# Optimization experiments

Measured on AMD Instinct MI355X. Metric: run time of the kernel, lower is better.

Reference implementation:

```python
import jax, jax.numpy as jnp
import numpy as np

EPS = 1e-4  # epsilon init kwarg


def setup_inputs() -> dict:
    key = jax.random.key(0)
    a = jax.random.normal(key, (8192, 64, 64), dtype=jnp.float32)
    # module assumes symmetric input (tf.self_adjoint_eig)
    x = 0.5 * (a + a.transpose(0, 2, 1))
    return {"x": x}


def reference(x):
    # batched symmetric eigendecomposition
    s, u = jnp.linalg.eigh(x)            # s: [b, d], u: [b, d, d]
    s = jnp.maximum(s, EPS)              # eigenvalue ReLU with shift epsilon
    # reconstruct: u @ diag(s) @ u^T
    return jnp.einsum('bik,bk,bjk->bij', u, s, u)
```

## Files before the change

### kernel.cpp

```cpp
#include <hip/hip_runtime.h>
#include <cstdint>


#define EPSV 1e-4f

typedef short bf16x8  __attribute__((ext_vector_type(8)));
typedef short short4v __attribute__((ext_vector_type(4)));
typedef float f32x4   __attribute__((ext_vector_type(4)));

__device__ __forceinline__ short f2bf(float f) {
  unsigned u = __float_as_uint(f);
  return (short)((u + 0x7FFFu + ((u >> 16) & 1u)) >> 16);
}
__device__ __forceinline__ float bf2f(short s) {
  return __uint_as_float(((unsigned)(unsigned short)s) << 16);
}
__device__ __forceinline__ int swz(int row, int byte) { return byte ^ ((row & 7) << 4); }

__device__ __forceinline__ bf16x8 ldfrag(const short* S, int row, int kb) {
  return *(const bf16x8*)((const char*)S + swz(row, row * 128 + kb));
}

__device__ __forceinline__ float blockReduceSum(float v, float* red) {
  #pragma unroll
  for (int o = 32; o >= 1; o >>= 1) v += __shfl_xor(v, o, 64);
  const int t = threadIdx.x;
  __syncthreads();
  if ((t & 63) == 0) red[t >> 6] = v;
  __syncthreads();
  return red[0] + red[1] + red[2] + red[3];
}

__device__ __forceinline__ void mm_split(const short* Ph, const short* Pl,
                                         const short* Qh, const short* Ql,
                                         int Rb, int Cb, int l15, int kg,
                                         f32x4 acc[2][2]) {
  #pragma unroll
  for (int mi = 0; mi < 2; mi++)
    #pragma unroll
    for (int ni = 0; ni < 2; ni++) acc[mi][ni] = (f32x4){0.f, 0.f, 0.f, 0.f};
  #pragma unroll
  for (int ks = 0; ks < 2; ks++) {
    const int kb = 64 * ks + 16 * kg;
    bf16x8 ah0 = ldfrag(Ph, Rb + l15,      kb);
    bf16x8 ah1 = ldfrag(Ph, Rb + 16 + l15, kb);
    bf16x8 al0 = ldfrag(Pl, Rb + l15,      kb);
    bf16x8 al1 = ldfrag(Pl, Rb + 16 + l15, kb);
    bf16x8 bh0 = ldfrag(Qh, Cb + l15,      kb);
    bf16x8 bh1 = ldfrag(Qh, Cb + 16 + l15, kb);
    bf16x8 bl0 = ldfrag(Ql, Cb + l15,      kb);
    bf16x8 bl1 = ldfrag(Ql, Cb + 16 + l15, kb);
#define MM(mi, ni, A, B) acc[mi][ni] = __builtin_amdgcn_mfma_f32_16x16x32_bf16(A, B, acc[mi][ni], 0, 0, 0)
    MM(0,0,ah0,bh0); MM(0,0,ah0,bl0); MM(0,0,al0,bh0);
    MM(0,1,ah0,bh1); MM(0,1,ah0,bl1); MM(0,1,al0,bh1);
    MM(1,0,ah1,bh0); MM(1,0,ah1,bl0); MM(1,0,al1,bh0);
    MM(1,1,ah1,bh1); MM(1,1,ah1,bl1); MM(1,1,al1,bh1);
#undef MM
  }
}

__device__ __forceinline__ void writeSym(short* Dh, short* Dl, const f32x4 vals[2][2],
                                         int Rb, int Cb, int l15, int kg, float scale) {
  #pragma unroll
  for (int mi = 0; mi < 2; mi++)
    #pragma unroll
    for (int ni = 0; ni < 2; ni++) {
      const int rp = Cb + 16 * ni + l15;
      const int cb2 = (Rb + 16 * mi + 4 * kg) * 2;
      short4v h, l;
      #pragma unroll
      for (int r = 0; r < 4; r++) {
        float v = vals[mi][ni][r] * scale;
        short hh = f2bf(v);
        h[r] = hh;
        l[r] = f2bf(v - bf2f(hh));
      }
      const int off = swz(rp, rp * 128 + cb2);
      *(short4v*)((char*)Dh + off) = h;
      *(short4v*)((char*)Dl + off) = l;
    }
}

__device__ __forceinline__ void readSym(const short* Sh, const short* Sl,
                                        int Rb, int Cb, int l15, int kg,
                                        f32x4 out[2][2]) {
  #pragma unroll
  for (int mi = 0; mi < 2; mi++)
    #pragma unroll
    for (int ni = 0; ni < 2; ni++) {
      const int rp = Cb + 16 * ni + l15;
      const int off = swz(rp, rp * 128 + (Rb + 16 * mi + 4 * kg) * 2);
      short4v h = *(const short4v*)((const char*)Sh + off);
      short4v l = *(const short4v*)((const char*)Sl + off);
      #pragma unroll
      for (int r = 0; r < 4; r++) out[mi][ni][r] = bf2f(h[r]) + bf2f(l[r]);
    }
}

__global__ __launch_bounds__(256, 2) void mrelu_mfma(const float* __restrict__ X,
                                                     float* __restrict__ O) {
  __shared__ short Yh[4096], Yl[4096], Zh[4096], Zl[4096],
                   Uh[4096], Ul[4096], Wh[4096], Wl[4096];
  __shared__ float red[4];

  const int t = threadIdx.x;
  const int lane = t & 63, wid = t >> 6;
  const int l15 = lane & 15, kg = lane >> 4;
  const int Rb = (wid >> 1) * 32, Cb = (wid & 1) * 32;
  const size_t base = (size_t)blockIdx.x * 4096;
  const float* Xb = X + base;

  float4 ld[4];
  float ssq = 0.f;
  #pragma unroll
  for (int q = 0; q < 4; q++) {
    float4 v = reinterpret_cast<const float4*>(Xb)[t + 256 * q];
    const int e = 4 * t + 1024 * q;
    const int row = e >> 6, col = e & 63;
    const int d = row - col;
    if (d >= 0 && d < 4) (&v.x)[d] -= EPSV;
    ssq += v.x * v.x + v.y * v.y + v.z * v.z + v.w * v.w;
    ld[q] = v;
  }
  const float s0sq = blockReduceSum(ssq, red);
  const float S0 = sqrtf(s0sq) + 1e-30f;
  const float invS0 = 1.0f / S0;

  #pragma unroll
  for (int q = 0; q < 4; q++) {
    const int e = 4 * t + 1024 * q;
    const int row = e >> 6, col = e & 63;
    short4v h, l;
    #pragma unroll
    for (int i = 0; i < 4; i++) {
      float v = (&ld[q].x)[i] * invS0;
      short hh = f2bf(v);
      h[i] = hh;
      l[i] = f2bf(v - bf2f(hh));
    }
    const int off = swz(row, row * 128 + col * 2);
    *(short4v*)((char*)Yh + off) = h;
    *(short4v*)((char*)Yl + off) = l;
  }
  __syncthreads();

  f32x4 acc[2][2];
  mm_split(Yh, Yl, Yh, Yl, Rb, Cb, l15, kg, acc);
  float zss = 0.f;
  #pragma unroll
  for (int mi = 0; mi < 2; mi++)
    #pragma unroll
    for (int ni = 0; ni < 2; ni++)
      #pragma unroll
      for (int r = 0; r < 4; r++) zss += acc[mi][ni][r] * acc[mi][ni][r];
  const float znSq = blockReduceSum(zss, red);
  const float rr = sqrtf(sqrtf(znSq + 1e-30f));
  const float invr = 1.0f / rr;
  const float S = S0 * rr;
  writeSym(Zh, Zl, acc, Rb, Cb, l15, kg, invr * invr);

  {
    f32x4 yv[2][2];
    readSym(Yh, Yl, Rb, Cb, l15, kg, yv);
    #pragma unroll
    for (int mi = 0; mi < 2; mi++)
      #pragma unroll
      for (int ni = 0; ni < 2; ni++)
        #pragma unroll
        for (int r = 0; r < 4; r++) yv[mi][ni][r] *= invr;
    writeSym(Yh, Yl, yv, Rb, Cb, l15, kg, 1.0f);
    writeSym(Wh, Wl, yv, Rb, Cb, l15, kg, 1.0f);
  }
  __syncthreads();

  const float qa = 3.4445f, qb = -4.7750f, qc = 2.0315f;
  #pragma unroll 1
  for (int it = 0; it < 4; it++) {
    mm_split(Zh, Zl, Yh, Yl, Rb, Cb, l15, kg, acc);
    writeSym(Uh, Ul, acc, Rb, Cb, l15, kg, 1.0f);
    __syncthreads();
    mm_split(Zh, Zl, Uh, Ul, Rb, Cb, l15, kg, acc);
    f32x4 yv[2][2], uv[2][2];
    readSym(Yh, Yl, Rb, Cb, l15, kg, yv);
    readSym(Uh, Ul, Rb, Cb, l15, kg, uv);
    f32x4 res[2][2];
    #pragma unroll
    for (int mi = 0; mi < 2; mi++)
      #pragma unroll
      for (int ni = 0; ni < 2; ni++)
        #pragma unroll
        for (int r = 0; r < 4; r++)
          res[mi][ni][r] = qa * yv[mi][ni][r] + qb * uv[mi][ni][r] + qc * acc[mi][ni][r];
    writeSym(Yh, Yl, res, Rb, Cb, l15, kg, 1.0f);
    __syncthreads();
    mm_split(Yh, Yl, Yh, Yl, Rb, Cb, l15, kg, acc);
    writeSym(Zh, Zl, acc, Rb, Cb, l15, kg, 1.0f);
    __syncthreads();
  }

  #pragma unroll 1
  for (int it = 0; it < 3; it++) {
    mm_split(Zh, Zl, Yh, Yl, Rb, Cb, l15, kg, acc);
    f32x4 yv[2][2];
    readSym(Yh, Yl, Rb, Cb, l15, kg, yv);
    __syncthreads();
    f32x4 res[2][2];
    #pragma unroll
    for (int mi = 0; mi < 2; mi++)
      #pragma unroll
      for (int ni = 0; ni < 2; ni++)
        #pragma unroll
        for (int r = 0; r < 4; r++)
          res[mi][ni][r] = 1.5f * yv[mi][ni][r] - 0.5f * acc[mi][ni][r];
    writeSym(Yh, Yl, res, Rb, Cb, l15, kg, 1.0f);
    __syncthreads();
    if (it < 2) {
      mm_split(Yh, Yl, Yh, Yl, Rb, Cb, l15, kg, acc);
      writeSym(Zh, Zl, acc, Rb, Cb, l15, kg, 1.0f);
      __syncthreads();
    }
  }

  mm_split(Wh, Wl, Yh, Yl, Rb, Cb, l15, kg, acc);
  f32x4 wv[2][2];
  readSym(Wh, Wl, Rb, Cb, l15, kg, wv);
  float* Ob = O + base;
  const float hS = 0.5f * S;
  #pragma unroll
  for (int mi = 0; mi < 2; mi++)
    #pragma unroll
    for (int ni = 0; ni < 2; ni++) {
      const int rp = Cb + 16 * ni + l15;
      const int cb = Rb + 16 * mi + 4 * kg;
      float4 o;
      #pragma unroll
      for (int r = 0; r < 4; r++)
        (&o.x)[r] = hS * (wv[mi][ni][r] + acc[mi][ni][r]) + ((rp == cb + r) ? EPSV : 0.f);
      *reinterpret_cast<float4*>(&Ob[rp * 64 + cb]) = o;
    }
}

extern "C" void kernel_launch(void* const* d_in, const int* in_sizes, int n_in,
                              void* d_out, int out_size, void* d_ws, size_t ws_size,
                              hipStream_t stream) {
  const float* X = (const float*)d_in[0];
  float* O = (float*)d_out;
  const int nmat = in_sizes[0] >> 12;
  mrelu_mfma<<<nmat, 256, 0, stream>>>(X, O);
}
```

Baseline: 517.7 us.

## Assign one matrix per wavefront with 32x32 MFMA and algebraically restructured iterations

Each wavefront now processes a whole 64x64 matrix in its own LDS region, so block-wide barriers and LDS reductions give way to wave shuffles and compiler fences. The matmuls use 32x32x16 bf16 MFMA with all fragments held in registers. The Newton-Schulz iterations are rewritten in polynomial form so identity terms are folded in via the diagonal, which removes the extra U and W buffers and the readback of the old Y. The final step recomputes X from global memory rather than keeping a W copy. Each wave does four times the work serially with large register pressure at launch bounds of 1, which may lower occupancy and lengthen latency per block.

```diff
diff --git a/kernel.cpp b/kernel.cpp
--- a/kernel.cpp
+++ b/kernel.cpp
@@ -6,7 +6,7 @@
 
 typedef short bf16x8  __attribute__((ext_vector_type(8)));
 typedef short short4v __attribute__((ext_vector_type(4)));
-typedef float f32x4   __attribute__((ext_vector_type(4)));
+typedef float f32x16  __attribute__((ext_vector_type(16)));
 
 __device__ __forceinline__ short f2bf(float f) {
   unsigned u = __float_as_uint(f);
@@ -16,227 +16,245 @@
   return __uint_as_float(((unsigned)(unsigned short)s) << 16);
 }
 __device__ __forceinline__ int swz(int row, int byte) { return byte ^ ((row & 7) << 4); }
-
-__device__ __forceinline__ bf16x8 ldfrag(const short* S, int row, int kb) {
-  return *(const bf16x8*)((const char*)S + swz(row, row * 128 + kb));
-}
-
-__device__ __forceinline__ float blockReduceSum(float v, float* red) {
-  #pragma unroll
-  for (int o = 32; o >= 1; o >>= 1) v += __shfl_xor(v, o, 64);
-  const int t = threadIdx.x;
-  __syncthreads();
-  if ((t & 63) == 0) red[t >> 6] = v;
-  __syncthreads();
-  return red[0] + red[1] + red[2] + red[3];
-}
-
-__device__ __forceinline__ void mm_split(const short* Ph, const short* Pl,
-                                         const short* Qh, const short* Ql,
-                                         int Rb, int Cb, int l15, int kg,
-                                         f32x4 acc[2][2]) {
-  #pragma unroll
-  for (int mi = 0; mi < 2; mi++)
-    #pragma unroll
-    for (int ni = 0; ni < 2; ni++) acc[mi][ni] = (f32x4){0.f, 0.f, 0.f, 0.f};
-  #pragma unroll
-  for (int ks = 0; ks < 2; ks++) {
-    const int kb = 64 * ks + 16 * kg;
-    bf16x8 ah0 = ldfrag(Ph, Rb + l15,      kb);
-    bf16x8 ah1 = ldfrag(Ph, Rb + 16 + l15, kb);
-    bf16x8 al0 = ldfrag(Pl, Rb + l15,      kb);
-    bf16x8 al1 = ldfrag(Pl, Rb + 16 + l15, kb);
-    bf16x8 bh0 = ldfrag(Qh, Cb + l15,      kb);
-    bf16x8 bh1 = ldfrag(Qh, Cb + 16 + l15, kb);
-    bf16x8 bl0 = ldfrag(Ql, Cb + l15,      kb);
-    bf16x8 bl1 = ldfrag(Ql, Cb + 16 + l15, kb);
-#define MM(mi, ni, A, B) acc[mi][ni] = __builtin_amdgcn_mfma_f32_16x16x32_bf16(A, B, acc[mi][ni], 0, 0, 0)
-    MM(0,0,ah0,bh0); MM(0,0,ah0,bl0); MM(0,0,al0,bh0);
-    MM(0,1,ah0,bh1); MM(0,1,ah0,bl1); MM(0,1,al0,bh1);
-    MM(1,0,ah1,bh0); MM(1,0,ah1,bl0); MM(1,0,al1,bh0);
-    MM(1,1,ah1,bh1); MM(1,1,ah1,bl1); MM(1,1,al1,bh1);
+__device__ __forceinline__ void fence() { __asm volatile("" ::: "memory"); }
+
+struct Frags { bf16x8 f[2][4]; };
+
+__device__ __forceinline__ void loadFrags(const short* buf, int l31, int h, Frags& F) {
+  #pragma unroll
+  for (int mi = 0; mi < 2; mi++)
+    #pragma unroll
+    for (int ks = 0; ks < 4; ks++) {
+      const int row = 32 * mi + l31;
+      F.f[mi][ks] = *(const bf16x8*)((const char*)buf + swz(row, row * 128 + 32 * ks + 16 * h));
+    }
+}
+
+__device__ __forceinline__ void chains3(const Frags& Ah, const Frags& Al,
+                                        const Frags& Bh, const Frags& Bl,
+                                        f32x16 acc[2][2]) {
+  #pragma unroll
+  for (int mi = 0; mi < 2; mi++)
+    #pragma unroll
+    for (int ni = 0; ni < 2; ni++)
+      #pragma unroll
+      for (int e = 0; e < 16; e++) acc[mi][ni][e] = 0.f;
+#define MM(A, B) acc[mi][ni] = __builtin_amdgcn_mfma_f32_32x32x16_bf16(A, B, acc[mi][ni], 0, 0, 0)
+  #pragma unroll
+  for (int ks = 0; ks < 4; ks++) {
+    #pragma unroll
+    for (int mi = 0; mi < 2; mi++)
+      #pragma unroll
+      for (int ni = 0; ni < 2; ni++) MM(Ah.f[mi][ks], Bh.f[ni][ks]);
+    #pragma unroll
+    for (int mi = 0; mi < 2; mi++)
+      #pragma unroll
+      for (int ni = 0; ni < 2; ni++) MM(Ah.f[mi][ks], Bl.f[ni][ks]);
+    #pragma unroll
+    for (int mi = 0; mi < 2; mi++)
+      #pragma unroll
+      for (int ni = 0; ni < 2; ni++) MM(Al.f[mi][ks], Bh.f[ni][ks]);
+  }
 #undef MM
-  }
-}
-
-__device__ __forceinline__ void writeSym(short* Dh, short* Dl, const f32x4 vals[2][2],
-                                         int Rb, int Cb, int l15, int kg, float scale) {
+}
+
+__device__ __forceinline__ void writeCT(short* bh, short* bl, const f32x16 acc[2][2],
+                                        int l31, int h, float scale) {
   #pragma unroll
   for (int mi = 0; mi < 2; mi++)
     #pragma unroll
     for (int ni = 0; ni < 2; ni++) {
-      const int rp = Cb + 16 * ni + l15;
-      const int cb2 = (Rb + 16 * mi + 4 * kg) * 2;
-      short4v h, l;
-      #pragma unroll
-      for (int r = 0; r < 4; r++) {
-        float v = vals[mi][ni][r] * scale;
-        short hh = f2bf(v);
-        h[r] = hh;
-        l[r] = f2bf(v - bf2f(hh));
+      const int R = 32 * ni + l31;
+      #pragma unroll
+      for (int q = 0; q < 4; q++) {
+        short4v hv, lv;
+        #pragma unroll
+        for (int p = 0; p < 4; p++) {
+          float v = acc[mi][ni][4 * q + p] * scale;
+          short hh = f2bf(v);
+          hv[p] = hh;
+          lv[p] = f2bf(v - bf2f(hh));
+        }
+        const int off = swz(R, R * 128 + (32 * mi + 8 * q + 4 * h) * 2);
+        *(short4v*)((char*)bh + off) = hv;
+        *(short4v*)((char*)bl + off) = lv;
       }
-      const int off = swz(rp, rp * 128 + cb2);
-      *(short4v*)((char*)Dh + off) = h;
-      *(short4v*)((char*)Dl + off) = l;
-    }
-}
-
-__device__ __forceinline__ void readSym(const short* Sh, const short* Sl,
-                                        int Rb, int Cb, int l15, int kg,
-                                        f32x4 out[2][2]) {
-  #pragma unroll
-  for (int mi = 0; mi < 2; mi++)
-    #pragma unroll
-    for (int ni = 0; ni < 2; ni++) {
-      const int rp = Cb + 16 * ni + l15;
-      const int off = swz(rp, rp * 128 + (Rb + 16 * mi + 4 * kg) * 2);
-      short4v h = *(const short4v*)((const char*)Sh + off);
-      short4v l = *(const short4v*)((const char*)Sl + off);
-      #pragma unroll
-      for (int r = 0; r < 4; r++) out[mi][ni][r] = bf2f(h[r]) + bf2f(l[r]);
-    }
-}
-
-__global__ __launch_bounds__(256, 2) void mrelu_mfma(const float* __restrict__ X,
-                                                     float* __restrict__ O) {
-  __shared__ short Yh[4096], Yl[4096], Zh[4096], Zl[4096],
-                   Uh[4096], Ul[4096], Wh[4096], Wl[4096];
-  __shared__ float red[4];
-
-  const int t = threadIdx.x;
-  const int lane = t & 63, wid = t >> 6;
-  const int l15 = lane & 15, kg = lane >> 4;
-  const int Rb = (wid >> 1) * 32, Cb = (wid & 1) * 32;
-  const size_t base = (size_t)blockIdx.x * 4096;
-  const float* Xb = X + base;
-
-  float4 ld[4];
+    }
+}
+
+__global__ __launch_bounds__(256, 1) void mrelu_w(const float* __restrict__ X,
+                                                  float* __restrict__ O, int nmat) {
+  __shared__ short lds[4][16384];
+  const int t = threadIdx.x, wid = t >> 6, l = t & 63;
+  const int l31 = l & 31, h = l >> 5;
+  const int mat = blockIdx.x * 4 + wid;
+  if (mat >= nmat) return;
+  const float* Xb = X + (size_t)mat * 4096;
+  short* Yh = &lds[wid][0];
+  short* Yl = Yh + 4096;
+  short* Zh = Yh + 8192;
+  short* Zl = Yh + 12288;
+
+  float4 xv[16];
   float ssq = 0.f;
   #pragma unroll
-  for (int q = 0; q < 4; q++) {
-    float4 v = reinterpret_cast<const float4*>(Xb)[t + 256 * q];
-    const int e = 4 * t + 1024 * q;
-    const int row = e >> 6, col = e & 63;
-    const int d = row - col;
+  for (int q = 0; q < 16; q++) {
+    float4 v = reinterpret_cast<const float4*>(Xb)[l + 64 * q];
+    const int e = 4 * l + 256 * q, row = e >> 6, col = e & 63, d = row - col;
     if (d >= 0 && d < 4) (&v.x)[d] -= EPSV;
     ssq += v.x * v.x + v.y * v.y + v.z * v.z + v.w * v.w;
-    ld[q] = v;
-  }
-  const float s0sq = blockReduceSum(ssq, red);
-  const float S0 = sqrtf(s0sq) + 1e-30f;
+    xv[q] = v;
+  }
+  #pragma unroll
+  for (int o = 32; o >= 1; o >>= 1) ssq += __shfl_xor(ssq, o, 64);
+  const float S0 = sqrtf(ssq) + 1e-30f;
   const float invS0 = 1.0f / S0;
 
   #pragma unroll
-  for (int q = 0; q < 4; q++) {
-    const int e = 4 * t + 1024 * q;
-    const int row = e >> 6, col = e & 63;
-    short4v h, l;
+  for (int q = 0; q < 16; q++) {
+    const int e = 4 * l + 256 * q, row = e >> 6, col = e & 63;
+    short4v hv, lv;
     #pragma unroll
     for (int i = 0; i < 4; i++) {
-      float v = (&ld[q].x)[i] * invS0;
+      float v = (&xv[q].x)[i] * invS0;
       short hh = f2bf(v);
-      h[i] = hh;
-      l[i] = f2bf(v - bf2f(hh));
+      hv[i] = hh;
+      lv[i] = f2bf(v - bf2f(hh));
     }
     const int off = swz(row, row * 128 + col * 2);
-    *(short4v*)((char*)Yh + off) = h;
-    *(short4v*)((char*)Yl + off) = l;
-  }
-  __syncthreads();
-
-  f32x4 acc[2][2];
-  mm_split(Yh, Yl, Yh, Yl, Rb, Cb, l15, kg, acc);
+    *(short4v*)((char*)Yh + off) = hv;
+    *(short4v*)((char*)Yl + off) = lv;
+  }
+  fence();
+
+  Frags FA, FB, FC, FD;
+  f32x16 accA[2][2], accB[2][2];
+
+  loadFrags(Yh, l31, h, FA);
+  loadFrags(Yl, l31, h, FB);
+  chains3(FA, FB, FA, FB, accA);
   float zss = 0.f;
   #pragma unroll
   for (int mi = 0; mi < 2; mi++)
     #pragma unroll
     for (int ni = 0; ni < 2; ni++)
       #pragma unroll
-      for (int r = 0; r < 4; r++) zss += acc[mi][ni][r] * acc[mi][ni][r];
-  const float znSq = blockReduceSum(zss, red);
-  const float rr = sqrtf(sqrtf(znSq + 1e-30f));
-  const float invr = 1.0f / rr;
-  const float S = S0 * rr;
-  writeSym(Zh, Zl, acc, Rb, Cb, l15, kg, invr * invr);
-
-  {
-    f32x4 yv[2][2];
-    readSym(Yh, Yl, Rb, Cb, l15, kg, yv);
-    #pragma unroll
-    for (int mi = 0; mi < 2; mi++)
-      #pragma unroll
-      for (int ni = 0; ni < 2; ni++)
-        #pragma unroll
-        for (int r = 0; r < 4; r++) yv[mi][ni][r] *= invr;
-    writeSym(Yh, Yl, yv, Rb, Cb, l15, kg, 1.0f);
-    writeSym(Wh, Wl, yv, Rb, Cb, l15, kg, 1.0f);
-  }
-  __syncthreads();
+      for (int e = 0; e < 16; e++) zss += accA[mi][ni][e] * accA[mi][ni][e];
+  #pragma unroll
+  for (int o = 32; o >= 1; o >>= 1) zss += __shfl_xor(zss, o, 64);
+  const float rr = sqrtf(sqrtf(zss + 1e-30f));
+  float lam = 1.0f / rr;
+  const float lam2 = lam * lam;
+  #pragma unroll
+  for (int mi = 0; mi < 2; mi++)
+    #pragma unroll
+    for (int ni = 0; ni < 2; ni++)
+      #pragma unroll
+      for (int e = 0; e < 16; e++) accA[mi][ni][e] *= lam2;
+  writeCT(Zh, Zl, accA, l31, h, 1.0f);
+  fence();
 
   const float qa = 3.4445f, qb = -4.7750f, qc = 2.0315f;
+
   #pragma unroll 1
   for (int it = 0; it < 4; it++) {
-    mm_split(Zh, Zl, Yh, Yl, Rb, Cb, l15, kg, acc);
-    writeSym(Uh, Ul, acc, Rb, Cb, l15, kg, 1.0f);
-    __syncthreads();
-    mm_split(Zh, Zl, Uh, Ul, Rb, Cb, l15, kg, acc);
-    f32x4 yv[2][2], uv[2][2];
-    readSym(Yh, Yl, Rb, Cb, l15, kg, yv);
-    readSym(Uh, Ul, Rb, Cb, l15, kg, uv);
-    f32x4 res[2][2];
+    if (it > 0) {
+      loadFrags(Yh, l31, h, FA);
+      loadFrags(Yl, l31, h, FB);
+      chains3(FA, FB, FA, FB, accA);
+      writeCT(Zh, Zl, accA, l31, h, 1.0f);
+      fence();
+    }
+    loadFrags(Zh, l31, h, FC);
+    loadFrags(Zl, l31, h, FD);
+    chains3(FC, FD, FC, FD, accB);
     #pragma unroll
     for (int mi = 0; mi < 2; mi++)
       #pragma unroll
       for (int ni = 0; ni < 2; ni++)
         #pragma unroll
-        for (int r = 0; r < 4; r++)
-          res[mi][ni][r] = qa * yv[mi][ni][r] + qb * uv[mi][ni][r] + qc * acc[mi][ni][r];
-    writeSym(Yh, Yl, res, Rb, Cb, l15, kg, 1.0f);
-    __syncthreads();
-    mm_split(Yh, Yl, Yh, Yl, Rb, Cb, l15, kg, acc);
-    writeSym(Zh, Zl, acc, Rb, Cb, l15, kg, 1.0f);
-    __syncthreads();
+        for (int r = 0; r < 16; r++) {
+          const int grow = 32 * mi + (r & 3) + 8 * (r >> 2) + 4 * h;
+          const int gcol = 32 * ni + l31;
+          accB[mi][ni][r] = qc * accB[mi][ni][r] + qb * accA[mi][ni][r] +
+                            ((grow == gcol) ? qa : 0.f);
+        }
+    writeCT(Zh, Zl, accB, l31, h, 1.0f);
+    fence();
+    loadFrags(Yh, l31, h, FA);
+    loadFrags(Yl, l31, h, FB);
+    loadFrags(Zh, l31, h, FC);
+    loadFrags(Zl, l31, h, FD);
+    chains3(FA, FB, FC, FD, accA);
+    writeCT(Yh, Yl, accA, l31, h, lam);
+    lam = 1.0f;
+    fence();
   }
 
   #pragma unroll 1
   for (int it = 0; it < 3; it++) {
-    mm_split(Zh, Zl, Yh, Yl, Rb, Cb, l15, kg, acc);
-    f32x4 yv[2][2];
-    readSym(Yh, Yl, Rb, Cb, l15, kg, yv);
-    __syncthreads();
-    f32x4 res[2][2];
+    loadFrags(Yh, l31, h, FA);
+    loadFrags(Yl, l31, h, FB);
+    chains3(FA, FB, FA, FB, accA);
     #pragma unroll
     for (int mi = 0; mi < 2; mi++)
       #pragma unroll
       for (int ni = 0; ni < 2; ni++)
         #pragma unroll
-        for (int r = 0; r < 4; r++)
-          res[mi][ni][r] = 1.5f * yv[mi][ni][r] - 0.5f * acc[mi][ni][r];
-    writeSym(Yh, Yl, res, Rb, Cb, l15, kg, 1.0f);
-    __syncthreads();
-    if (it < 2) {
-      mm_split(Yh, Yl, Yh, Yl, Rb, Cb, l15, kg, acc);
-      writeSym(Zh, Zl, acc, Rb, Cb, l15, kg, 1.0f);
-      __syncthreads();
-    }
-  }
-
-  mm_split(Wh, Wl, Yh, Yl, Rb, Cb, l15, kg, acc);
-  f32x4 wv[2][2];
-  readSym(Wh, Wl, Rb, Cb, l15, kg, wv);
-  float* Ob = O + base;
-  const float hS = 0.5f * S;
+        for (int r = 0; r < 16; r++) {
+          const int grow = 32 * mi + (r & 3) + 8 * (r >> 2) + 4 * h;
+          const int gcol = 32 * ni + l31;
+          accA[mi][ni][r] = ((grow == gcol) ? 1.5f : 0.f) - 0.5f * accA[mi][ni][r];
+        }
+    writeCT(Zh, Zl, accA, l31, h, 1.0f);
+    fence();
+    loadFrags(Zh, l31, h, FC);
+    loadFrags(Zl, l31, h, FD);
+    chains3(FA, FB, FC, FD, accB);
+    writeCT(Yh, Yl, accB, l31, h, 1.0f);
+    fence();
+  }
+
+  loadFrags(Yh, l31, h, FA);
+  loadFrags(Yl, l31, h, FB);
+  #pragma unroll
+  for (int mi = 0; mi < 2; mi++)
+    #pragma unroll
+    for (int ks = 0; ks < 4; ks++) {
+      const int row = 32 * mi + l31;
+      const int k0 = 16 * ks + 8 * h;
+      float4 a = *reinterpret_cast<const float4*>(&Xb[row * 64 + k0]);
+      float4 b = *reinterpret_cast<const float4*>(&Xb[row * 64 + k0 + 4]);
+      bf16x8 hh, ll;
+      #pragma unroll
+      for (int j = 0; j < 8; j++) {
+        float v = (j < 4) ? (&a.x)[j] : (&b.x)[j - 4];
+        if (row == k0 + j) v -= EPSV;
+        short hb = f2bf(v);
+        hh[j] = hb;
+        ll[j] = f2bf(v - bf2f(hb));
+      }
+      FC.f[mi][ks] = hh;
+      FD.f[mi][ks] = ll;
+    }
+  chains3(FC, FD, FA, FB, accA);
+  float* Ob = O + (size_t)mat * 4096;
   #pragma unroll
   for (int mi = 0; mi < 2; mi++)
     #pragma unroll
     for (int ni = 0; ni < 2; ni++) {
-      const int rp = Cb + 16 * ni + l15;
-      const int cb = Rb + 16 * mi + 4 * kg;
-      float4 o;
-      #pragma unroll
-      for (int r = 0; r < 4; r++)
-        (&o.x)[r] = hS * (wv[mi][ni][r] + acc[mi][ni][r]) + ((rp == cb + r) ? EPSV : 0.f);
-      *reinterpret_cast<float4*>(&Ob[rp * 64 + cb]) = o;
+      const int R = 32 * ni + l31;
+      #pragma unroll
+      for (int q = 0; q < 4; q++) {
+        const int cb = 32 * mi + 8 * q + 4 * h;
+        float4 x = *reinterpret_cast<const float4*>(&Xb[R * 64 + cb]);
+        float4 o;
+        #pragma unroll
+        for (int p = 0; p < 4; p++)
+          (&o.x)[p] = 0.5f * (&x.x)[p] + 0.5f * accA[mi][ni][4 * q + p] +
+                      ((R == cb + p) ? 0.5f * EPSV : 0.f);
+        *reinterpret_cast<float4*>(&Ob[R * 64 + cb]) = o;
+      }
     }
 }
 
@@ -246,5 +264,6 @@
   const float* X = (const float*)d_in[0];
   float* O = (float*)d_out;
   const int nmat = in_sizes[0] >> 12;
-  mrelu_mfma<<<nmat, 256, 0, stream>>>(X, O);
-}
+  const int blocks = (nmat + 3) / 4;
+  mrelu_w<<<blocks, 256, 0, stream>>>(X, O, nmat);
+}
```

Result: slower. 581.8 us (+12.4%).
